# Kernel tuning notes

Hardware: AMD Instinct MI355X
Metric: run time of the kernel (lower is better)

The kernel has to match this reference:

```python
import jax, jax.numpy as jnp
import numpy as np

D_MODEL = 1024
N_HEADS = 16
D_HEAD = D_MODEL // N_HEADS

def setup_inputs() -> dict:
    key = jax.random.key(0)
    ks = jax.random.split(key, 5)
    B, T = 4, 2048
    s = 1.0 / np.sqrt(D_MODEL)
    return {
        "x": jax.random.normal(ks[0], (B, T, D_MODEL), dtype=jnp.float32),
        "qkv_w": jax.random.normal(ks[1], (3 * D_MODEL, D_MODEL), dtype=jnp.float32) * s,
        "qkv_b": jnp.zeros((3 * D_MODEL,), dtype=jnp.float32),
        "out_w": jax.random.normal(ks[2], (D_MODEL, D_MODEL), dtype=jnp.float32) * s,
        "out_b": jnp.zeros((D_MODEL,), dtype=jnp.float32),
    }

def reference(x, qkv_w, qkv_b, out_w, out_b):
    B, T, D = x.shape
    # fused QKV projection: [B,T,3D] -> [3,B,H,T,dh]
    qkv = (x @ qkv_w.T + qkv_b).reshape(B, T, 3, N_HEADS, D_HEAD)
    qkv = jnp.transpose(qkv, (2, 0, 3, 1, 4))
    q, k, v = qkv[0], qkv[1], qkv[2]
    scale = 1.0 / np.sqrt(D_HEAD).astype(np.float32)
    scores = jnp.einsum("bhqd,bhkd->bhqk", q, k) * scale
    attn = jax.nn.softmax(scores, axis=-1)
    ctx = jnp.einsum("bhqk,bhkd->bhqd", attn, v)  # [B,H,T,dh]
    ctx = jnp.transpose(ctx, (0, 2, 1, 3)).reshape(B, T, D)
    return ctx @ out_w.T + out_b
```

## Files before the change

### kernel.cpp

```cpp
#include <hip/hip_runtime.h>
#include <hip/hip_bf16.h>
#include <cstdint>
#include <cstddef>


#define SEQ 2048
#define DM 1024

typedef __attribute__((ext_vector_type(8))) short bf16x8;
typedef __attribute__((ext_vector_type(4))) short bf16x4;
typedef __attribute__((ext_vector_type(4))) float f32x4;

static __device__ __forceinline__ short f2bf(float f) {
  union { float f; uint32_t u; } v; v.f = f;
  uint32_t r = v.u + 0x7fffu + ((v.u >> 16) & 1u);
  return (short)(r >> 16);
}

typedef const __attribute__((address_space(1))) unsigned int* gas_ptr;
typedef __attribute__((address_space(3))) unsigned int* las_ptr;
static __device__ __forceinline__ void gl2lds16(const void* g, void* l) {
  __builtin_amdgcn_global_load_lds((gas_ptr)g, (las_ptr)l, 16, 0, 0);
}

static __device__ __forceinline__ bf16x8 pack8(const float* p) {
  union { bf16x8 v; __hip_bfloat162 h[4]; } u;
#pragma unroll
  for (int i = 0; i < 4; i++) {
    float2 f2; f2.x = p[2 * i]; f2.y = p[2 * i + 1];
    u.h[i] = __float22bfloat162_rn(f2);
  }
  return u.v;
}

static __device__ __forceinline__ int swz(int r) {
  return (r & 3) | (((r >> 3) & 1) << 2);
}

__global__ __launch_bounds__(256)
void cvt_bf16(const float* __restrict__ src, short* __restrict__ dst) {
  int i = blockIdx.x * 256 + threadIdx.x;
  float4 v = ((const float4*)src)[i];
  bf16x4 p = { f2bf(v.x), f2bf(v.y), f2bf(v.z), f2bf(v.w) };
  ((bf16x4*)dst)[i] = p;
}

__global__ __launch_bounds__(256, 2)
void qkv_gemm(const short* __restrict__ Xb, const short* __restrict__ Wb,
              const float* __restrict__ bias,
              short* __restrict__ Q, short* __restrict__ K,
              short* __restrict__ Vt) {
  __shared__ short As[128][64];
  __shared__ short Bs[128][64];
  const int tid  = threadIdx.x;
  const int m0   = blockIdx.x * 128;
  const int n0   = blockIdx.y * 128;
  const int lane = tid & 63;
  const int w    = tid >> 6;
  const int wm   = (w >> 1) * 64, wn = (w & 1) * 64;
  const int l15  = lane & 15, quad = lane >> 4;
  const int arow = w * 8 + (lane >> 3), acol = (lane & 7) << 3;

  f32x4 acc[4][4];
  for (int i = 0; i < 4; i++)
    for (int j = 0; j < 4; j++) acc[i][j] = (f32x4)0.0f;

  for (int k0 = 0; k0 < DM; k0 += 64) {
#pragma unroll
    for (int p = 0; p < 4; p++) {
      gl2lds16(&Xb[(size_t)(m0 + p * 32 + arow) * DM + k0 + acol], &As[p * 32 + w * 8][0]);
      gl2lds16(&Wb[(size_t)(n0 + p * 32 + arow) * DM + k0 + acol], &Bs[p * 32 + w * 8][0]);
    }
    __syncthreads();
#pragma unroll
    for (int ks = 0; ks < 64; ks += 32) {
      bf16x8 af[4], bfr[4];
      for (int i = 0; i < 4; i++)
        af[i] = *(const bf16x8*)&As[wm + i * 16 + l15][ks + quad * 8];
      for (int j = 0; j < 4; j++)
        bfr[j] = *(const bf16x8*)&Bs[wn + j * 16 + l15][ks + quad * 8];
      for (int i = 0; i < 4; i++)
        for (int j = 0; j < 4; j++)
          acc[i][j] = __builtin_amdgcn_mfma_f32_16x16x32_bf16(af[i], bfr[j], acc[i][j], 0, 0, 0);
    }
    __syncthreads();
  }

  const float C1 = 0.18033688011112042f;
  const int qkv = n0 >> 10;
  for (int i = 0; i < 4; i++) {
    const int m = m0 + wm + i * 16 + quad * 4;
    const int bb = m >> 11, t = m & 2047;
    for (int j = 0; j < 4; j++) {
      const int f  = n0 + wn + j * 16 + l15;
      const int fi = f & 1023;
      const int h  = fi >> 6, d = fi & 63;
      const float bv = bias[f];
      if (qkv == 2) {
        bf16x4 pk = { f2bf(acc[i][j][0] + bv), f2bf(acc[i][j][1] + bv),
                      f2bf(acc[i][j][2] + bv), f2bf(acc[i][j][3] + bv) };
        *(bf16x4*)&Vt[((size_t)(bb * 16 + h) * 64 + d) * SEQ + t] = pk;
      } else {
        short* dst = (qkv == 0) ? Q : K;
        const float sc = (qkv == 0) ? C1 : 1.0f;
        size_t base = ((size_t)(bb * 16 + h) * SEQ + t) * 64 + d;
        for (int r = 0; r < 4; r++)
          dst[base + (size_t)r * 64] = f2bf((acc[i][j][r] + bv) * sc);
      }
    }
  }
}

__global__ __launch_bounds__(256, 4)
void attn(const short* __restrict__ Q, const short* __restrict__ K,
          const short* __restrict__ Vt, short* __restrict__ ctx) {
  __shared__ short Ks[2][64 * 64];
  __shared__ short Vs[2][64 * 64];
  const int tid  = threadIdx.x;
  const int w    = tid >> 6, lane = tid & 63;
  const int l15  = lane & 15, quad = lane >> 4;
  const int bh   = blockIdx.y;
  const int qr   = blockIdx.x * 128 + w * 32;
  const short* Kb = &K[(size_t)bh * SEQ * 64];
  const short* Vb = &Vt[(size_t)bh * 64 * SEQ];

  const int kperm = (l15 >> 2) * 8 + (l15 & 3);

  int dr[2], dc[2];
#pragma unroll
  for (int p = 0; p < 2; p++) {
    int ci = p * 256 + w * 64 + lane;
    dr[p] = ci >> 3;
    dc[p] = (ci & 7) ^ swz(ci >> 3);
  }

  bf16x8 qf[2][2];
#pragma unroll
  for (int mt = 0; mt < 2; mt++)
#pragma unroll
    for (int ks = 0; ks < 2; ks++)
      qf[mt][ks] = *(const bf16x8*)&Q[(size_t)bh * SEQ * 64 + (size_t)(qr + mt * 16 + l15) * 64 + ks * 32 + quad * 8];

  f32x4 O[2][4];
#pragma unroll
  for (int mt = 0; mt < 2; mt++)
    for (int dt = 0; dt < 4; dt++) O[mt][dt] = (f32x4)0.0f;
  f32x4 psA[2];
  psA[0] = (f32x4)0.0f; psA[1] = (f32x4)0.0f;
  const short one_bf = (short)0x3F80;
  const bf16x8 ones = { one_bf, one_bf, one_bf, one_bf, one_bf, one_bf, one_bf, one_bf };

#pragma unroll
  for (int p = 0; p < 2; p++) {
    gl2lds16(&Kb[(size_t)dr[p] * 64 + dc[p] * 8],  &Ks[0][(p * 256 + w * 64) * 8]);
    gl2lds16(&Vb[(size_t)dr[p] * SEQ + dc[p] * 8], &Vs[0][(p * 256 + w * 64) * 8]);
  }
  __syncthreads();

  int it = 0;
  for (int k0 = 0; k0 < SEQ; k0 += 64, it ^= 1) {
    if (k0 + 64 < SEQ) {
      const int kn = k0 + 64;
#pragma unroll
      for (int p = 0; p < 2; p++) {
        gl2lds16(&Kb[(size_t)(kn + dr[p]) * 64 + dc[p] * 8], &Ks[it ^ 1][(p * 256 + w * 64) * 8]);
        gl2lds16(&Vb[(size_t)dr[p] * SEQ + kn + dc[p] * 8],  &Vs[it ^ 1][(p * 256 + w * 64) * 8]);
      }
    }

    bf16x8 kf[2][2][2];
#pragma unroll
    for (int blk = 0; blk < 2; blk++)
#pragma unroll
      for (int tau = 0; tau < 2; tau++)
#pragma unroll
        for (int ks = 0; ks < 2; ks++) {
          int R = blk * 32 + kperm + tau * 4;
          int c = (ks * 4 + quad) ^ swz(R);
          kf[blk][tau][ks] = *(const bf16x8*)&Ks[it][(R * 8 + c) * 8];
        }

    f32x4 S[2][2][2];
#pragma unroll
    for (int mt = 0; mt < 2; mt++)
#pragma unroll
      for (int blk = 0; blk < 2; blk++) {
        f32x4 S0 = (f32x4)0.0f, S1 = (f32x4)0.0f;
#pragma unroll
        for (int ks = 0; ks < 2; ks++) {
          S0 = __builtin_amdgcn_mfma_f32_16x16x32_bf16(kf[blk][0][ks], qf[mt][ks], S0, 0, 0, 0);
          S1 = __builtin_amdgcn_mfma_f32_16x16x32_bf16(kf[blk][1][ks], qf[mt][ks], S1, 0, 0, 0);
        }
        S[mt][blk][0] = S0; S[mt][blk][1] = S1;
      }

    bf16x8 vf[4][2];
#pragma unroll
    for (int dt = 0; dt < 4; dt++)
#pragma unroll
      for (int blk = 0; blk < 2; blk++) {
        int R = dt * 16 + l15;
        int c = (blk * 4 + quad) ^ swz(R);
        vf[dt][blk] = *(const bf16x8*)&Vs[it][(R * 8 + c) * 8];
      }

    bf16x8 pp[2][2];
#pragma unroll
    for (int mt = 0; mt < 2; mt++)
#pragma unroll
      for (int blk = 0; blk < 2; blk++) {
        float e[8];
#pragma unroll
        for (int r = 0; r < 4; r++) {
          e[r]     = exp2f(S[mt][blk][0][r]);
          e[4 + r] = exp2f(S[mt][blk][1][r]);
        }
        pp[mt][blk] = pack8(e);
      }

#pragma unroll
    for (int blk = 0; blk < 2; blk++) {
#pragma unroll
      for (int dt = 0; dt < 4; dt++) {
        O[0][dt] = __builtin_amdgcn_mfma_f32_16x16x32_bf16(vf[dt][blk], pp[0][blk], O[0][dt], 0, 0, 0);
        O[1][dt] = __builtin_amdgcn_mfma_f32_16x16x32_bf16(vf[dt][blk], pp[1][blk], O[1][dt], 0, 0, 0);
      }
      psA[0] = __builtin_amdgcn_mfma_f32_16x16x32_bf16(ones, pp[0][blk], psA[0], 0, 0, 0);
      psA[1] = __builtin_amdgcn_mfma_f32_16x16x32_bf16(ones, pp[1][blk], psA[1], 0, 0, 0);
    }

    __syncthreads();
  }

  const int bb = bh >> 4, h = bh & 15;
#pragma unroll
  for (int mt = 0; mt < 2; mt++) {
    float rinv = 1.0f / psA[mt][0];
    const int t = qr + mt * 16 + l15;
#pragma unroll
    for (int dt = 0; dt < 4; dt++) {
      bf16x4 ov = { f2bf(O[mt][dt][0] * rinv), f2bf(O[mt][dt][1] * rinv),
                    f2bf(O[mt][dt][2] * rinv), f2bf(O[mt][dt][3] * rinv) };
      *(bf16x4*)&ctx[(size_t)(bb * SEQ + t) * DM + h * 64 + dt * 16 + quad * 4] = ov;
    }
  }
}

__global__ __launch_bounds__(256, 2)
void out_gemm(const short* __restrict__ Cx, const short* __restrict__ Ob,
              const float* __restrict__ bias, float* __restrict__ Y) {
  __shared__ short As[128][64];
  __shared__ short Bs[128][64];
  const int tid  = threadIdx.x;
  const int m0   = blockIdx.x * 128;
  const int n0   = blockIdx.y * 128;
  const int lane = tid & 63;
  const int w    = tid >> 6;
  const int wm   = (w >> 1) * 64, wn = (w & 1) * 64;
  const int l15  = lane & 15, quad = lane >> 4;
  const int arow = w * 8 + (lane >> 3), acol = (lane & 7) << 3;

  f32x4 acc[4][4];
  for (int i = 0; i < 4; i++)
    for (int j = 0; j < 4; j++) acc[i][j] = (f32x4)0.0f;

  for (int k0 = 0; k0 < DM; k0 += 64) {
#pragma unroll
    for (int p = 0; p < 4; p++) {
      gl2lds16(&Cx[(size_t)(m0 + p * 32 + arow) * DM + k0 + acol], &As[p * 32 + w * 8][0]);
      gl2lds16(&Ob[(size_t)(n0 + p * 32 + arow) * DM + k0 + acol], &Bs[p * 32 + w * 8][0]);
    }
    __syncthreads();
#pragma unroll
    for (int ks = 0; ks < 64; ks += 32) {
      bf16x8 af[4], bfr[4];
      for (int i = 0; i < 4; i++)
        af[i] = *(const bf16x8*)&As[wm + i * 16 + l15][ks + quad * 8];
      for (int j = 0; j < 4; j++)
        bfr[j] = *(const bf16x8*)&Bs[wn + j * 16 + l15][ks + quad * 8];
      for (int i = 0; i < 4; i++)
        for (int j = 0; j < 4; j++)
          acc[i][j] = __builtin_amdgcn_mfma_f32_16x16x32_bf16(af[i], bfr[j], acc[i][j], 0, 0, 0);
    }
    __syncthreads();
  }

  for (int i = 0; i < 4; i++) {
    const int m = m0 + wm + i * 16 + quad * 4;
    for (int j = 0; j < 4; j++) {
      const int n = n0 + wn + j * 16 + l15;
      const float bv = bias[n];
      for (int r = 0; r < 4; r++)
        Y[(size_t)(m + r) * DM + n] = acc[i][j][r] + bv;
    }
  }
}

extern "C" void kernel_launch(void* const* d_in, const int* in_sizes, int n_in,
                              void* d_out, int out_size, void* d_ws, size_t ws_size,
                              hipStream_t stream) {
  const float* x     = (const float*)d_in[0];
  const float* qkv_w = (const float*)d_in[1];
  const float* qkv_b = (const float*)d_in[2];
  const float* out_w = (const float*)d_in[3];
  const float* out_b = (const float*)d_in[4];
  float* out = (float*)d_out;

  const size_t NBH = (size_t)4 * 16 * SEQ * 64;
  short* Q   = (short*)d_ws;
  short* K   = Q + NBH;
  short* Vt  = K + NBH;
  short* ctx = Vt + NBH;
  short* Xb  = ctx;
  short* Ob  = Vt;
  short* Wb  = (short*)d_out;

  cvt_bf16<<<dim3(8192), 256, 0, stream>>>(x, Xb);
  cvt_bf16<<<dim3(3072), 256, 0, stream>>>(qkv_w, Wb);
  qkv_gemm<<<dim3(64, 24), 256, 0, stream>>>(Xb, Wb, qkv_b, Q, K, Vt);
  attn<<<dim3(SEQ / 128, 64), 256, 0, stream>>>(Q, K, Vt, ctx);
  cvt_bf16<<<dim3(1024), 256, 0, stream>>>(out_w, Ob);
  out_gemm<<<dim3(64, 8), 256, 0, stream>>>(ctx, Ob, out_b, out);
}
```

Measured before the change: 299.3 us.

## Unroll attention K-loop by two with precomputed LDS offsets and truncating bf16 pack

Unrolls the attention key loop by two so the double-buffer index is a compile-time constant. LDS fragment offsets and global prefetch pointers are precomputed outside the loop instead of being recomputed with swizzles each iteration. Replaces round-to-nearest bf16 packing of the softmax probabilities with a single byte-permute truncation, which costs some accuracy. Lowers the launch-bounds occupancy hint from 4 to 2 blocks per CU, giving the compiler more registers but risking less latency hiding.

```diff
diff --git a/kernel.cpp b/kernel.cpp
--- a/kernel.cpp
+++ b/kernel.cpp
@@ -23,14 +23,17 @@
   __builtin_amdgcn_global_load_lds((gas_ptr)g, (las_ptr)l, 16, 0, 0);
 }
 
-static __device__ __forceinline__ bf16x8 pack8(const float* p) {
-  union { bf16x8 v; __hip_bfloat162 h[4]; } u;
-#pragma unroll
-  for (int i = 0; i < 4; i++) {
-    float2 f2; f2.x = p[2 * i]; f2.y = p[2 * i + 1];
-    u.h[i] = __float22bfloat162_rn(f2);
-  }
-  return u.v;
+static __device__ __forceinline__ unsigned permhi(float a_odd, float a_even) {
+  union { float f; unsigned u; } x, y; x.f = a_odd; y.f = a_even;
+  return __builtin_amdgcn_perm(x.u, y.u, 0x07060302u);
+}
+static __device__ __forceinline__ bf16x8 pack8t(const float* e) {
+  union { bf16x8 v; unsigned u[4]; } r;
+  r.u[0] = permhi(e[1], e[0]);
+  r.u[1] = permhi(e[3], e[2]);
+  r.u[2] = permhi(e[5], e[4]);
+  r.u[3] = permhi(e[7], e[6]);
+  return r.v;
 }
 
 static __device__ __forceinline__ int swz(int r) {
@@ -111,7 +114,7 @@
   }
 }
 
-__global__ __launch_bounds__(256, 4)
+__global__ __launch_bounds__(256, 2)
 void attn(const short* __restrict__ Q, const short* __restrict__ K,
           const short* __restrict__ Vt, short* __restrict__ ctx) {
   __shared__ short Ks[2][64 * 64];
@@ -133,6 +136,40 @@
     dr[p] = ci >> 3;
     dc[p] = (ci & 7) ^ swz(ci >> 3);
   }
+  const short* kp[2];
+  const short* vp[2];
+#pragma unroll
+  for (int p = 0; p < 2; p++) {
+    kp[p] = &Kb[(size_t)(64 + dr[p]) * 64 + dc[p] * 8];
+    vp[p] = &Vb[(size_t)dr[p] * SEQ + 64 + dc[p] * 8];
+  }
+
+  int koff[2][2][2][2];
+  int voff[2][4][2];
+#pragma unroll
+  for (int blk = 0; blk < 2; blk++)
+#pragma unroll
+    for (int tau = 0; tau < 2; tau++)
+#pragma unroll
+      for (int ks = 0; ks < 2; ks++) {
+        int R = blk * 32 + kperm + tau * 4;
+        int c = (ks * 4 + quad) ^ swz(R);
+        int off = (R * 8 + c) * 16;
+        koff[0][blk][tau][ks] = off;
+        koff[1][blk][tau][ks] = off + 8192;
+      }
+#pragma unroll
+  for (int dt = 0; dt < 4; dt++)
+#pragma unroll
+    for (int blk = 0; blk < 2; blk++) {
+      int R = dt * 16 + l15;
+      int c = (blk * 4 + quad) ^ swz(R);
+      int off = (R * 8 + c) * 16;
+      voff[0][dt][blk] = off;
+      voff[1][dt][blk] = off + 8192;
+    }
+  const char* KsB = (const char*)&Ks[0][0];
+  const char* VsB = (const char*)&Vs[0][0];
 
   bf16x8 qf[2][2];
 #pragma unroll
@@ -157,79 +194,77 @@
   }
   __syncthreads();
 
-  int it = 0;
-  for (int k0 = 0; k0 < SEQ; k0 += 64, it ^= 1) {
-    if (k0 + 64 < SEQ) {
-      const int kn = k0 + 64;
-#pragma unroll
-      for (int p = 0; p < 2; p++) {
-        gl2lds16(&Kb[(size_t)(kn + dr[p]) * 64 + dc[p] * 8], &Ks[it ^ 1][(p * 256 + w * 64) * 8]);
-        gl2lds16(&Vb[(size_t)dr[p] * SEQ + kn + dc[p] * 8],  &Vs[it ^ 1][(p * 256 + w * 64) * 8]);
+  for (int k0 = 0; k0 < SEQ; k0 += 128) {
+#pragma unroll
+    for (int half = 0; half < 2; half++) {
+      const bool doPf = (half == 0) || (k0 + 128 < SEQ);
+      if (doPf) {
+#pragma unroll
+        for (int p = 0; p < 2; p++) {
+          gl2lds16(kp[p], &Ks[half ^ 1][(p * 256 + w * 64) * 8]);
+          gl2lds16(vp[p], &Vs[half ^ 1][(p * 256 + w * 64) * 8]);
+        }
       }
-    }
-
-    bf16x8 kf[2][2][2];
-#pragma unroll
-    for (int blk = 0; blk < 2; blk++)
-#pragma unroll
-      for (int tau = 0; tau < 2; tau++)
-#pragma unroll
-        for (int ks = 0; ks < 2; ks++) {
-          int R = blk * 32 + kperm + tau * 4;
-          int c = (ks * 4 + quad) ^ swz(R);
-          kf[blk][tau][ks] = *(const bf16x8*)&Ks[it][(R * 8 + c) * 8];
+#pragma unroll
+      for (int p = 0; p < 2; p++) { kp[p] += 64 * 64; vp[p] += 64; }
+
+      bf16x8 kf[2][2][2];
+#pragma unroll
+      for (int blk = 0; blk < 2; blk++)
+#pragma unroll
+        for (int tau = 0; tau < 2; tau++)
+#pragma unroll
+          for (int ks = 0; ks < 2; ks++)
+            kf[blk][tau][ks] = *(const bf16x8*)(KsB + koff[half][blk][tau][ks]);
+
+      f32x4 S[2][2][2];
+#pragma unroll
+      for (int mt = 0; mt < 2; mt++)
+#pragma unroll
+        for (int blk = 0; blk < 2; blk++) {
+          f32x4 S0 = (f32x4)0.0f, S1 = (f32x4)0.0f;
+#pragma unroll
+          for (int ks = 0; ks < 2; ks++) {
+            S0 = __builtin_amdgcn_mfma_f32_16x16x32_bf16(kf[blk][0][ks], qf[mt][ks], S0, 0, 0, 0);
+            S1 = __builtin_amdgcn_mfma_f32_16x16x32_bf16(kf[blk][1][ks], qf[mt][ks], S1, 0, 0, 0);
+          }
+          S[mt][blk][0] = S0; S[mt][blk][1] = S1;
         }
 
-    f32x4 S[2][2][2];
-#pragma unroll
-    for (int mt = 0; mt < 2; mt++)
+      bf16x8 vf[4][2];
+#pragma unroll
+      for (int dt = 0; dt < 4; dt++)
+#pragma unroll
+        for (int blk = 0; blk < 2; blk++)
+          vf[dt][blk] = *(const bf16x8*)(VsB + voff[half][dt][blk]);
+
+      bf16x8 pp[2][2];
+#pragma unroll
+      for (int mt = 0; mt < 2; mt++)
+#pragma unroll
+        for (int blk = 0; blk < 2; blk++) {
+          float e[8];
+#pragma unroll
+          for (int r = 0; r < 4; r++) {
+            e[r]     = exp2f(S[mt][blk][0][r]);
+            e[4 + r] = exp2f(S[mt][blk][1][r]);
+          }
+          pp[mt][blk] = pack8t(e);
+        }
+
 #pragma unroll
       for (int blk = 0; blk < 2; blk++) {
-        f32x4 S0 = (f32x4)0.0f, S1 = (f32x4)0.0f;
-#pragma unroll
-        for (int ks = 0; ks < 2; ks++) {
-          S0 = __builtin_amdgcn_mfma_f32_16x16x32_bf16(kf[blk][0][ks], qf[mt][ks], S0, 0, 0, 0);
-          S1 = __builtin_amdgcn_mfma_f32_16x16x32_bf16(kf[blk][1][ks], qf[mt][ks], S1, 0, 0, 0);
+#pragma unroll
+        for (int dt = 0; dt < 4; dt++) {
+          O[0][dt] = __builtin_amdgcn_mfma_f32_16x16x32_bf16(vf[dt][blk], pp[0][blk], O[0][dt], 0, 0, 0);
+          O[1][dt] = __builtin_amdgcn_mfma_f32_16x16x32_bf16(vf[dt][blk], pp[1][blk], O[1][dt], 0, 0, 0);
         }
-        S[mt][blk][0] = S0; S[mt][blk][1] = S1;
+        psA[0] = __builtin_amdgcn_mfma_f32_16x16x32_bf16(ones, pp[0][blk], psA[0], 0, 0, 0);
+        psA[1] = __builtin_amdgcn_mfma_f32_16x16x32_bf16(ones, pp[1][blk], psA[1], 0, 0, 0);
       }
 
-    bf16x8 vf[4][2];
-#pragma unroll
-    for (int dt = 0; dt < 4; dt++)
-#pragma unroll
-      for (int blk = 0; blk < 2; blk++) {
-        int R = dt * 16 + l15;
-        int c = (blk * 4 + quad) ^ swz(R);
-        vf[dt][blk] = *(const bf16x8*)&Vs[it][(R * 8 + c) * 8];
-      }
-
-    bf16x8 pp[2][2];
-#pragma unroll
-    for (int mt = 0; mt < 2; mt++)
-#pragma unroll
-      for (int blk = 0; blk < 2; blk++) {
-        float e[8];
-#pragma unroll
-        for (int r = 0; r < 4; r++) {
-          e[r]     = exp2f(S[mt][blk][0][r]);
-          e[4 + r] = exp2f(S[mt][blk][1][r]);
-        }
-        pp[mt][blk] = pack8(e);
-      }
-
-#pragma unroll
-    for (int blk = 0; blk < 2; blk++) {
-#pragma unroll
-      for (int dt = 0; dt < 4; dt++) {
-        O[0][dt] = __builtin_amdgcn_mfma_f32_16x16x32_bf16(vf[dt][blk], pp[0][blk], O[0][dt], 0, 0, 0);
-        O[1][dt] = __builtin_amdgcn_mfma_f32_16x16x32_bf16(vf[dt][blk], pp[1][blk], O[1][dt], 0, 0, 0);
-      }
-      psA[0] = __builtin_amdgcn_mfma_f32_16x16x32_bf16(ones, pp[0][blk], psA[0], 0, 0, 0);
-      psA[1] = __builtin_amdgcn_mfma_f32_16x16x32_bf16(ones, pp[1][blk], psA[1], 0, 0, 0);
-    }
-
-    __syncthreads();
+      __syncthreads();
+    }
   }
 
   const int bb = bh >> 4, h = bh & 15;
```

After: 289.0 us. 3.5% less time.
